# Performance work log

Hardware: AMD Instinct MI355X
Metric: run time of the kernel (lower is better)

## Reference

```python
import jax, jax.numpy as jnp
import numpy as np

L, B, S, E, H, V = 4, 2, 1024, 1024, 16, 32000
HD = E // H          # head_size = 64
FF = 6 * E           # FeedForward expansion = 6
EPS = 1e-5


def setup_inputs() -> dict:
    key = jax.random.key(0)
    ks = jax.random.split(key, 12)
    std = jnp.float32(0.02)

    def nrm(k, shape):
        return jax.random.normal(k, shape, jnp.float32) * std

    return {
        "x":   jax.random.randint(ks[0], (B, S), 0, V),
        "emb": nrm(ks[1], (V, E)),            # token embedding table
        "pos": nrm(ks[2], (S, E)),            # position embedding table (context = S)
        "Wq":  nrm(ks[3], (L, H, E, HD)),     # per-layer, per-head q Linear (no bias)
        "Wk":  nrm(ks[4], (L, H, E, HD)),
        "Wv":  nrm(ks[5], (L, H, E, HD)),
        "Wo":  nrm(ks[6], (L, E, E)),         # MHA output projection
        "g1":  jnp.ones((L, E), jnp.float32), "b1": jnp.zeros((L, E), jnp.float32),
        "g2":  jnp.ones((L, E), jnp.float32), "b2": jnp.zeros((L, E), jnp.float32),
        "W1":  nrm(ks[7], (L, E, FF)),        # FFN up
        "W2":  nrm(ks[8], (L, FF, E)),        # FFN down
        "gf":  jnp.ones((E,), jnp.float32), "bf": jnp.zeros((E,), jnp.float32),
        "Wf":  nrm(ks[9], (E, V)),            # final LM head (no bias)
    }


def _ln(x, g, b):
    mu = jnp.mean(x, -1, keepdims=True)
    var = jnp.mean((x - mu) ** 2, -1, keepdims=True)
    return (x - mu) * jax.lax.rsqrt(var + EPS) * g + b


def _gpt(x, emb, pos, Wq, Wk, Wv, Wo, g1, b1, g2, b2, W1, W2, gf, bf, Wf):
    Bsz, Sl = x.shape
    h = emb[x] + pos[:Sl]                         # [B,S,E]
    mask = jnp.tril(jnp.ones((Sl, Sl), bool))     # causal 'trill' buffer

    def block(h, p):
        wq, wk, wv, wo, ga, ba, gb, bb, w1, w2 = p
        z = _ln(h, ga, ba)
        q = jnp.einsum('bse,hed->bhsd', z, wq)
        k = jnp.einsum('bse,hed->bhsd', z, wk)
        v = jnp.einsum('bse,hed->bhsd', z, wv)
        att = jnp.einsum('bhsd,bhtd->bhst', q, k) * (HD ** -0.5)
        att = jnp.where(mask, att, -jnp.inf)
        att = jax.nn.softmax(att, axis=-1)
        o = jnp.einsum('bhst,bhtd->bhsd', att, v)
        o = o.transpose(0, 2, 1, 3).reshape(h.shape[0], h.shape[1], E)  # concat heads
        h = h + o @ wo                                                   # residual 1
        z = _ln(h, gb, bb)
        h = h + jax.nn.gelu(z @ w1, approximate=False) @ w2              # residual 2
        return h, None

    h, _ = jax.lax.scan(block, h, (Wq, Wk, Wv, Wo, g1, b1, g2, b2, W1, W2))
    return _ln(h, gf, bf) @ Wf                    # logits [B,S,V]


def reference(x, emb, pos, Wq, Wk, Wv, Wo, g1, b1, g2, b2, W1, W2, gf, bf, Wf):
    return _gpt(x, emb, pos, Wq, Wk, Wv, Wo, g1, b1, g2, b2, W1, W2, gf, bf, Wf)
```

## Files before the change

kernel.cpp:

```cpp
#include <hip/hip_runtime.h>
#include <hip/hip_bf16.h>
#include <math.h>


typedef unsigned short ushort_t;
typedef unsigned short us8 __attribute__((ext_vector_type(8)));
typedef unsigned short us4 __attribute__((ext_vector_type(4)));
typedef __bf16 bf16x8 __attribute__((ext_vector_type(8)));
typedef float f32x4 __attribute__((ext_vector_type(4)));

#define LN_EPS 1e-5f

__device__ inline ushort_t f2bf(float f) {
    union { float f; unsigned u; } v; v.f = f;
    unsigned r = v.u + 0x7FFFu + ((v.u >> 16) & 1u);
    return (ushort_t)(r >> 16);
}

#define GLD_LDS16(gp, lp)                                                  \
    __builtin_amdgcn_global_load_lds(                                      \
        (const __attribute__((address_space(1))) unsigned int*)(gp),       \
        (__attribute__((address_space(3))) unsigned int*)(lp), 16, 0, 0)

enum { EPI_F32 = 0, EPI_BF16 = 1, EPI_ADDF32 = 2, EPI_GELU = 3, EPI_TBF16 = 4,
       EPI_ATOM = 5, EPI_QKV = 6 };

template<int EPI>
__global__ __launch_bounds__(512)
void gemm8ph(const ushort_t* __restrict__ A, const ushort_t* __restrict__ B,
             void* __restrict__ Cv, int mt, int K, int lda, int ldb, int ldc)
{
    extern __shared__ ushort_t smem[];

    const int nwg  = gridDim.x;
    const int orig = blockIdx.x;
    int wgid = orig;
    if (nwg >= 8) {
        const int q = nwg >> 3, r = nwg & 7;
        const int xcd = orig & 7, i = orig >> 3;
        wgid = (xcd < r ? xcd * (q + 1) : r * (q + 1) + (xcd - r) * q) + i;
    }
    const int m0 = (wgid % mt) * 256;
    const int n0 = (wgid / mt) * 256;

    const int tid  = threadIdx.x;
    const int lane = tid & 63;
    const int wid  = tid >> 6;
    const int wm   = wid >> 2, wn = wid & 3;
    const int cg   = lane >> 4, cl = lane & 15;

    const int nt = K >> 6;
    const int ni = nt >> 1;

    auto stageA = [&](int t, int h) {
        ushort_t* dst = smem + (t & 1) * 32768 + h * 8192;
        const int k0 = t * 64;
        #pragma unroll
        for (int q = 0; q < 2; ++q) {
            const int slot = q * 512 + tid;
            const int r = slot >> 3, pc = slot & 7;
            const int col = (pc ^ (r & 7)) * 8;
            GLD_LDS16(&A[(long)(m0 + h * 128 + r) * lda + k0 + col], dst + slot * 8);
        }
    };
    auto stageB = [&](int t, int h) {
        ushort_t* dst = smem + (t & 1) * 32768 + 16384 + h * 8192;
        const int k0 = t * 64;
        #pragma unroll
        for (int q = 0; q < 2; ++q) {
            const int slot = q * 512 + tid;
            const int r = slot >> 3, pc = slot & 7;
            const int col = (pc ^ (r & 7)) * 8;
            GLD_LDS16(&B[(long)(n0 + h * 128 + r) * ldb + k0 + col], dst + slot * 8);
        }
    };

    stageA(0, 0); stageA(0, 1);
    stageB(0, 0); stageB(0, 1);
    stageB(1, 0); stageB(1, 1);
    asm volatile("s_waitcnt vmcnt(4)" ::: "memory");
    __builtin_amdgcn_s_barrier();

    f32x4 acc[8][4] = {};
    bf16x8 breg[4][2];

    for (int i = 0; i < ni; ++i) {
        const int te = 2 * i, to = te + 1;
        const bool nl = (i + 1 < ni);

        #pragma unroll
        for (int p = 0; p < 8; ++p) {
            const int t = (p < 4) ? te : to;
            const int q = p & 3;
            const ushort_t* Ar = smem + (t & 1) * 32768;
            const ushort_t* Br = Ar + 16384;

            if (q == 0) {
                #pragma unroll
                for (int nf = 0; nf < 4; ++nf) {
                    const int rb = wn * 64 + nf * 16 + cl;
                    #pragma unroll
                    for (int kk = 0; kk < 2; ++kk)
                        breg[nf][kk] = __builtin_bit_cast(bf16x8, *(const us8*)&Br[
                            rb * 64 + (((kk * 4 + cg) ^ (rb & 7)) * 8)]);
                }
            }
            bf16x8 af[2][2];
            #pragma unroll
            for (int mi = 0; mi < 2; ++mi) {
                const int ra = wm * 128 + q * 32 + mi * 16 + cl;
                #pragma unroll
                for (int kk = 0; kk < 2; ++kk)
                    af[mi][kk] = __builtin_bit_cast(bf16x8, *(const us8*)&Ar[
                        ra * 64 + (((kk * 4 + cg) ^ (ra & 7)) * 8)]);
            }

            if (p == 0)      { stageA(to, 0); }
            else if (p == 1) { stageA(to, 1); if (nl) stageB(te + 2, 0); }
            else if (p == 2) { if (nl) stageB(te + 2, 1); }
            else if (p == 4) { if (nl) stageA(te + 2, 0); }
            else if (p == 5) { if (nl) stageA(te + 2, 1); }
            else if (p == 6) { if (nl) stageB(to + 2, 0); }
            else if (p == 7) { if (nl) stageB(to + 2, 1); }

            __builtin_amdgcn_s_barrier();
            asm volatile("s_waitcnt lgkmcnt(0)" ::: "memory");
            __builtin_amdgcn_s_setprio(1);
            #pragma unroll
            for (int mi = 0; mi < 2; ++mi)
                #pragma unroll
                for (int nf = 0; nf < 4; ++nf)
                    #pragma unroll
                    for (int kk = 0; kk < 2; ++kk)
                        acc[q * 2 + mi][nf] = __builtin_amdgcn_mfma_f32_16x16x32_bf16(
                            af[mi][kk], breg[nf][kk], acc[q * 2 + mi][nf], 0, 0, 0);
            __builtin_amdgcn_s_setprio(0);

            if (p == 3) {
                if (nl) asm volatile("s_waitcnt vmcnt(4)" ::: "memory");
                else    asm volatile("s_waitcnt vmcnt(0)" ::: "memory");
            } else if (p == 7 && nl) {
                asm volatile("s_waitcnt vmcnt(4)" ::: "memory");
            }
            __builtin_amdgcn_s_barrier();
        }
    }

    const int rb = m0 + wm * 128 + cg * 4;
    const int cb = n0 + wn * 64 + cl;

    #pragma unroll
    for (int mf = 0; mf < 8; ++mf) {
        #pragma unroll
        for (int nf = 0; nf < 4; ++nf) {
            const int colg = cb + nf * 16;
            #pragma unroll
            for (int r = 0; r < 4; ++r) {
                const int  rowg = rb + mf * 16 + r;
                const long off  = (long)rowg * ldc + colg;
                const float val = acc[mf][nf][r];
                if (EPI == EPI_F32) {
                    ((float*)Cv)[off] = val;
                } else if (EPI == EPI_GELU) {
                    float g = 0.5f * val * (1.0f + erff(val * 0.70710678118654752f));
                    ((ushort_t*)Cv)[off] = f2bf(g);
                } else {
                    ((ushort_t*)Cv)[off] = f2bf(val);
                }
            }
        }
    }
}

template<int EPI>
__global__ __launch_bounds__(512)
void gemm8p(const ushort_t* __restrict__ A, const ushort_t* __restrict__ B,
            void* __restrict__ Cv, int mt, int K, int lda, int ldb, int ldc,
            long bsA, long bsB, long bsC)
{
    extern __shared__ ushort_t smem[];

    const int nwg  = gridDim.x;
    const int orig = blockIdx.x;
    int wgid = orig;
    if (nwg >= 8) {
        const int q = nwg >> 3, r = nwg & 7;
        const int xcd = orig & 7, i = orig >> 3;
        wgid = (xcd < r ? xcd * (q + 1) : r * (q + 1) + (xcd - r) * q) + i;
    }
    const int m0 = (wgid % mt) * 128;
    const int n0 = (wgid / mt) * 256;

    A += (long)blockIdx.z * bsA;
    B += (long)blockIdx.z * bsB;

    const int tid  = threadIdx.x;
    const int lane = tid & 63;
    const int wid  = tid >> 6;
    const int wm   = wid >> 2, wn = wid & 3;
    const int cg   = lane >> 4, cl = lane & 15;
    const int lr   = lane >> 3;
    const int lcc  = (lane & 7) * 8;

    const int nt = K >> 6;

    auto stage = [&](int kt, int buf, int part) {
        ushort_t* base = smem + buf * 24576;
        const int k0 = kt * 64;
        if (part < 2) {
            const int rbase = part * 64 + wid * 8;
            const int row   = rbase + lr;
            const int col   = lcc ^ ((row & 7) << 3);
            GLD_LDS16(&A[(long)(m0 + row) * lda + k0 + col], base + rbase * 64);
        } else {
            const int rbase = (part - 2) * 64 + wid * 8;
            const int row   = rbase + lr;
            const int col   = lcc ^ ((row & 7) << 3);
            GLD_LDS16(&B[(long)(n0 + row) * ldb + k0 + col],
                      base + 8192 + rbase * 64);
        }
    };

    #pragma unroll
    for (int p = 0; p < 6; ++p) stage(0, 0, p);
    #pragma unroll
    for (int p = 0; p < 6; ++p) stage(1, 1, p);
    asm volatile("s_waitcnt vmcnt(6)" ::: "memory");
    __builtin_amdgcn_s_barrier();

    f32x4 acc[4][4] = {};

    for (int t = 0; t < nt; ++t) {
        const ushort_t* Aq = smem + (t % 3) * 24576;
        const ushort_t* Bq = Aq + 8192;
        const int sbuf = (t + 2) % 3;
        const bool do_stage = (t + 2 < nt);

        bf16x8 breg[4][2];
        #pragma unroll
        for (int p = 0; p < 4; ++p) {
            const int rowA = wm * 64 + p * 16 + cl;
            bf16x8 aA[2];
            #pragma unroll
            for (int kk = 0; kk < 2; ++kk)
                aA[kk] = __builtin_bit_cast(bf16x8, *(const us8*)&Aq[
                    rowA * 64 + ((kk * 32 + cg * 8) ^ ((rowA & 7) << 3))]);
            if (p == 0) {
                #pragma unroll
                for (int nj = 0; nj < 4; ++nj) {
                    const int rowB = wn * 64 + nj * 16 + cl;
                    #pragma unroll
                    for (int kk = 0; kk < 2; ++kk)
                        breg[nj][kk] = __builtin_bit_cast(bf16x8, *(const us8*)&Bq[
                            rowB * 64 + ((kk * 32 + cg * 8) ^ ((rowB & 7) << 3))]);
                }
            }
            if (do_stage) {
                if (p == 0)      { stage(t + 2, sbuf, 0); stage(t + 2, sbuf, 1); }
                else if (p == 1) { stage(t + 2, sbuf, 2); stage(t + 2, sbuf, 3); }
                else if (p == 2) { stage(t + 2, sbuf, 4); }
                else             { stage(t + 2, sbuf, 5); }
            }
            __builtin_amdgcn_s_setprio(1);
            #pragma unroll
            for (int nj = 0; nj < 4; ++nj)
                #pragma unroll
                for (int kk = 0; kk < 2; ++kk)
                    acc[p][nj] = __builtin_amdgcn_mfma_f32_16x16x32_bf16(
                        aA[kk], breg[nj][kk], acc[p][nj], 0, 0, 0);
            __builtin_amdgcn_s_setprio(0);
            __builtin_amdgcn_s_barrier();
        }
        if (do_stage) asm volatile("s_waitcnt vmcnt(6)" ::: "memory");
        else          asm volatile("s_waitcnt vmcnt(0)" ::: "memory");
        __builtin_amdgcn_s_barrier();
    }

    const int rb = m0 + wm * 64 + cg * 4;
    const int cb = n0 + wn * 64 + cl;

    #pragma unroll
    for (int mi = 0; mi < 4; ++mi) {
        #pragma unroll
        for (int nj = 0; nj < 4; ++nj) {
            const int colg = cb + nj * 16;
            if (EPI == EPI_QKV) {
                ushort_t* Q = (ushort_t*)Cv;
                if (n0 < 1024) {
                    #pragma unroll
                    for (int r = 0; r < 4; ++r)
                        Q[(long)(rb + mi * 16 + r) * 1024 + colg] = f2bf(acc[mi][nj][r]);
                } else if (n0 < 2048) {
                    #pragma unroll
                    for (int r = 0; r < 4; ++r)
                        Q[2097152 + (long)(rb + mi * 16 + r) * 1024 + (colg - 1024)] =
                            f2bf(acc[mi][nj][r]);
                } else {
                    ushort_t* Vt = Q + 4194304;
                    const int rowg = rb + mi * 16;
                    const long boff = (long)(rowg >> 10) * 1048576;
                    us4 o4;
                    #pragma unroll
                    for (int r = 0; r < 4; ++r) o4[r] = f2bf(acc[mi][nj][r]);
                    *(us4*)&Vt[boff + (long)(colg - 2048) * 1024 + (rowg & 1023)] = o4;
                }
            } else {
                #pragma unroll
                for (int r = 0; r < 4; ++r) {
                    const int  rowg = rb + mi * 16 + r;
                    const long off  = (long)rowg * ldc + colg;
                    const float val = acc[mi][nj][r];
                    if (EPI == EPI_F32) {
                        ((float*)Cv)[off] = val;
                    } else if (EPI == EPI_GELU) {
                        float g = 0.5f * val * (1.0f + erff(val * 0.70710678118654752f));
                        ((ushort_t*)Cv)[off] = f2bf(g);
                    } else if (EPI == EPI_ATOM) {
                        atomicAdd(&((float*)Cv)[off], val);
                    } else {
                        ((ushort_t*)Cv)[off] = f2bf(val);
                    }
                }
            }
        }
    }
}

template<int EPI, int MT>
__global__ __launch_bounds__(256)
void gemm128(const ushort_t* __restrict__ A, const ushort_t* __restrict__ B,
             void* __restrict__ Cv, int K, int lda, int ldb, int ldc)
{
    const int m0 = blockIdx.x * (MT * 32);
    const int n0 = blockIdx.y * 128;

    __shared__ __align__(16) ushort_t As[MT * 32][64];
    __shared__ __align__(16) ushort_t Bs[128][64];

    const int tid  = threadIdx.x;
    const int lane = tid & 63;
    const int wid  = tid >> 6;
    const int wr   = wid >> 1, wc = wid & 1;
    const int lr   = lane >> 3;
    const int lc   = (lane & 7) * 8;
    const int cg   = lane >> 4;
    const int cl   = lane & 15;

    f32x4 acc[MT][4] = {};

    for (int k0 = 0; k0 < K; k0 += 64) {
        #pragma unroll
        for (int j = 0; j < MT; ++j) {
            const int r = wid * (8 * MT) + j * 8;
            GLD_LDS16(&A[(long)(m0 + r + lr) * lda + k0 + lc], &As[r][0]);
        }
        #pragma unroll
        for (int j = 0; j < 4; ++j) {
            const int r = wid * 32 + j * 8;
            GLD_LDS16(&B[(long)(n0 + r + lr) * ldb + k0 + lc], &Bs[r][0]);
        }
        __syncthreads();
        #pragma unroll
        for (int kk = 0; kk < 2; ++kk) {
            const int krd = kk * 32 + cg * 8;
            bf16x8 af[MT], bfr[4];
            #pragma unroll
            for (int mi = 0; mi < MT; ++mi)
                af[mi] = __builtin_bit_cast(bf16x8,
                    *(const us8*)&As[wr * (MT * 16) + mi * 16 + cl][krd]);
            #pragma unroll
            for (int nj = 0; nj < 4; ++nj)
                bfr[nj] = __builtin_bit_cast(bf16x8,
                    *(const us8*)&Bs[wc * 64 + nj * 16 + cl][krd]);
            #pragma unroll
            for (int mi = 0; mi < MT; ++mi)
                #pragma unroll
                for (int nj = 0; nj < 4; ++nj)
                    acc[mi][nj] = __builtin_amdgcn_mfma_f32_16x16x32_bf16(
                        af[mi], bfr[nj], acc[mi][nj], 0, 0, 0);
        }
        __syncthreads();
    }

    const int rb = m0 + wr * (MT * 16) + cg * 4;
    const int cb = n0 + wc * 64 + cl;

    #pragma unroll
    for (int mi = 0; mi < MT; ++mi)
        #pragma unroll
        for (int nj = 0; nj < 4; ++nj)
            #pragma unroll
            for (int r = 0; r < 4; ++r) {
                const long off = (long)(rb + mi * 16 + r) * ldc + cb + nj * 16;
                const float val = acc[mi][nj][r];
                if (EPI == EPI_ADDF32)      ((float*)Cv)[off] += val;
                else if (EPI == EPI_F32)    ((float*)Cv)[off] = val;
                else                        ((ushort_t*)Cv)[off] = f2bf(val);
            }
}

__global__ __launch_bounds__(256)
void flash_attn(const ushort_t* __restrict__ qb, const ushort_t* __restrict__ kb,
                const ushort_t* __restrict__ vT, ushort_t* __restrict__ ob)
{
    const int qt = gridDim.x - 1 - blockIdx.x;
    const int hh = blockIdx.y;
    const int bb = blockIdx.z;
    const int lane = threadIdx.x & 63;
    const int w    = threadIdx.x >> 6;
    const int cg   = lane >> 4;
    const int cl   = lane & 15;

    __shared__ __align__(16) ushort_t P_lds[4][16][72];

    const int q0 = qt * 64;
    const long tokQ = (long)bb * 1024 + q0 + w * 16 + cl;

    bf16x8 qf[2];
    #pragma unroll
    for (int kk = 0; kk < 2; ++kk)
        qf[kk] = __builtin_bit_cast(bf16x8,
            *(const us8*)&qb[tokQ * 1024 + hh * 64 + kk * 32 + cg * 8]);

    const ushort_t* kbase = kb + (long)bb * 1048576 + hh * 64;
    const ushort_t* vbase = vT + (long)bb * 1048576 + (long)hh * 65536;

    f32x4 o[4] = {};
    float m4[4], l4[4];
    #pragma unroll
    for (int r = 0; r < 4; ++r) { m4[r] = -1e30f; l4[r] = 0.0f; }

    for (int tt = 0; tt <= qt; ++tt) {
        const int t0 = tt * 64;
        f32x4 s[4] = {};
        __builtin_amdgcn_s_setprio(1);
        #pragma unroll
        for (int nj = 0; nj < 4; ++nj) {
            const ushort_t* kp = kbase + (long)(t0 + nj * 16 + cl) * 1024 + cg * 8;
            bf16x8 kf0 = __builtin_bit_cast(bf16x8, *(const us8*)kp);
            bf16x8 kf1 = __builtin_bit_cast(bf16x8, *(const us8*)(kp + 32));
            s[nj] = __builtin_amdgcn_mfma_f32_16x16x32_bf16(qf[0], kf0, s[nj], 0, 0, 0);
            s[nj] = __builtin_amdgcn_mfma_f32_16x16x32_bf16(qf[1], kf1, s[nj], 0, 0, 0);
        }
        __builtin_amdgcn_s_setprio(0);
        const bool diag = (tt == qt);
        float pm[4] = {-3e30f, -3e30f, -3e30f, -3e30f};
        #pragma unroll
        for (int nj = 0; nj < 4; ++nj)
            #pragma unroll
            for (int r = 0; r < 4; ++r) {
                float v = s[nj][r] * 0.125f;
                if (diag && (t0 + nj * 16 + cl) > (q0 + w * 16 + cg * 4 + r))
                    v = -1e30f;
                s[nj][r] = v;
                pm[r] = fmaxf(pm[r], v);
            }
        #pragma unroll
        for (int r = 0; r < 4; ++r)
            #pragma unroll
            for (int msk = 1; msk < 16; msk <<= 1)
                pm[r] = fmaxf(pm[r], __shfl_xor(pm[r], msk));
        float al[4], ps[4];
        #pragma unroll
        for (int r = 0; r < 4; ++r) {
            const float mn = fmaxf(m4[r], pm[r]);
            al[r] = __expf(m4[r] - mn);
            m4[r] = mn;
            ps[r] = 0.0f;
        }
        #pragma unroll
        for (int nj = 0; nj < 4; ++nj)
            #pragma unroll
            for (int r = 0; r < 4; ++r) {
                const float p = __expf(s[nj][r] - m4[r]);
                s[nj][r] = p;
                ps[r] += p;
            }
        #pragma unroll
        for (int r = 0; r < 4; ++r) {
            #pragma unroll
            for (int msk = 1; msk < 16; msk <<= 1)
                ps[r] += __shfl_xor(ps[r], msk);
            l4[r] = l4[r] * al[r] + ps[r];
        }
        #pragma unroll
        for (int nj = 0; nj < 4; ++nj)
            #pragma unroll
            for (int r = 0; r < 4; ++r) o[nj][r] *= al[r];
        #pragma unroll
        for (int nj = 0; nj < 4; ++nj)
            #pragma unroll
            for (int r = 0; r < 4; ++r)
                P_lds[w][cg * 4 + r][nj * 16 + cl] = f2bf(s[nj][r]);
        asm volatile("s_waitcnt lgkmcnt(0)" ::: "memory");
        __builtin_amdgcn_sched_barrier(0);
        bf16x8 pa[2];
        #pragma unroll
        for (int kk = 0; kk < 2; ++kk)
            pa[kk] = __builtin_bit_cast(bf16x8,
                *(const us8*)&P_lds[w][cl][kk * 32 + cg * 8]);
        __builtin_amdgcn_s_setprio(1);
        #pragma unroll
        for (int nj = 0; nj < 4; ++nj) {
            const ushort_t* vp = vbase + (long)(nj * 16 + cl) * 1024 + t0 + cg * 8;
            bf16x8 vf0 = __builtin_bit_cast(bf16x8, *(const us8*)vp);
            bf16x8 vf1 = __builtin_bit_cast(bf16x8, *(const us8*)(vp + 32));
            o[nj] = __builtin_amdgcn_mfma_f32_16x16x32_bf16(pa[0], vf0, o[nj], 0, 0, 0);
            o[nj] = __builtin_amdgcn_mfma_f32_16x16x32_bf16(pa[1], vf1, o[nj], 0, 0, 0);
        }
        __builtin_amdgcn_s_setprio(0);
    }

    #pragma unroll
    for (int r = 0; r < 4; ++r) {
        const float inv = 1.0f / l4[r];
        const long tok = (long)bb * 1024 + q0 + w * 16 + cg * 4 + r;
        #pragma unroll
        for (int nj = 0; nj < 4; ++nj)
            ob[tok * 1024 + hh * 64 + nj * 16 + cl] = f2bf(o[nj][r] * inv);
    }
}

__global__ __launch_bounds__(256)
void transpose_conv(const float* __restrict__ in, ushort_t* __restrict__ out,
                    long ldin, long ldout, long bsin, long bsout,
                    long bsout_hi, int zmod)
{
    __shared__ float tile[32][33];
    const int tx = threadIdx.x, ty = threadIdx.y;
    const long bin  = (long)blockIdx.z * bsin;
    const long bout = (long)(blockIdx.z % zmod) * bsout
                    + (long)(blockIdx.z / zmod) * bsout_hi;
    const int n0 = blockIdx.x * 32, k0 = blockIdx.y * 32;
    #pragma unroll
    for (int i = 0; i < 4; ++i)
        tile[ty + i * 8][tx] = in[bin + (long)(k0 + ty + i * 8) * ldin + n0 + tx];
    __syncthreads();
    #pragma unroll
    for (int i = 0; i < 4; ++i) {
        const int n = ty + i * 8;
        out[bout + (long)(n0 + n) * ldout + k0 + tx] = f2bf(tile[tx][n]);
    }
}

__global__ __launch_bounds__(256)
void embed_kernel(const int* __restrict__ x, const float* __restrict__ emb,
                  const float* __restrict__ pos, float* __restrict__ h)
{
    const int row = blockIdx.x, tid = threadIdx.x;
    const int s = row & 1023;
    const int idx = x[row];
    const float4 e = ((const float4*)(emb + (long)idx * 1024))[tid];
    const float4 p = ((const float4*)(pos + (long)s * 1024))[tid];
    float4 o; o.x = e.x + p.x; o.y = e.y + p.y; o.z = e.z + p.z; o.w = e.w + p.w;
    ((float4*)(h + (long)row * 1024))[tid] = o;
}

__global__ __launch_bounds__(256)
void ln_kernel(const float* __restrict__ x, const float* __restrict__ g,
               const float* __restrict__ b, ushort_t* __restrict__ z)
{
    const int row = blockIdx.x, tid = threadIdx.x;
    const float4 v = ((const float4*)(x + (long)row * 1024))[tid];
    float s  = v.x + v.y + v.z + v.w;
    float sq = v.x * v.x + v.y * v.y + v.z * v.z + v.w * v.w;
    #pragma unroll
    for (int o = 32; o > 0; o >>= 1) { s += __shfl_down(s, o); sq += __shfl_down(sq, o); }
    __shared__ float ls[4], lq[4];
    if ((tid & 63) == 0) { ls[tid >> 6] = s; lq[tid >> 6] = sq; }
    __syncthreads();
    s  = ls[0] + ls[1] + ls[2] + ls[3];
    sq = lq[0] + lq[1] + lq[2] + lq[3];
    const float mu   = s * (1.0f / 1024.0f);
    const float var  = sq * (1.0f / 1024.0f) - mu * mu;
    const float rstd = rsqrtf(var + LN_EPS);
    const float4 gg = ((const float4*)g)[tid];
    const float4 bb = ((const float4*)b)[tid];
    us4 o4;
    o4[0] = f2bf((v.x - mu) * rstd * gg.x + bb.x);
    o4[1] = f2bf((v.y - mu) * rstd * gg.y + bb.y);
    o4[2] = f2bf((v.z - mu) * rstd * gg.z + bb.z);
    o4[3] = f2bf((v.w - mu) * rstd * gg.w + bb.w);
    *(us4*)(z + (long)row * 1024 + tid * 4) = o4;
}

extern "C" void kernel_launch(void* const* d_in, const int* in_sizes, int n_in,
                              void* d_out, int out_size, void* d_ws, size_t ws_size,
                              hipStream_t stream)
{
    const int*   x   = (const int*)  d_in[0];
    const float* emb = (const float*)d_in[1];
    const float* pos = (const float*)d_in[2];
    const float* Wq  = (const float*)d_in[3];
    const float* Wk  = (const float*)d_in[4];
    const float* Wv  = (const float*)d_in[5];
    const float* Wo  = (const float*)d_in[6];
    const float* g1  = (const float*)d_in[7];
    const float* b1  = (const float*)d_in[8];
    const float* g2  = (const float*)d_in[9];
    const float* b2  = (const float*)d_in[10];
    const float* W1  = (const float*)d_in[11];
    const float* W2  = (const float*)d_in[12];
    const float* gf  = (const float*)d_in[13];
    const float* bfp = (const float*)d_in[14];
    const float* Wf  = (const float*)d_in[15];
    float* out = (float*)d_out;

    char* ws = (char*)d_ws;
    size_t off = 0;
    auto alloc = [&](size_t bytes) {
        char* p = ws + off;
        off = (off + bytes + 255) & ~(size_t)255;
        return p;
    };
    ushort_t* WqkvT = (ushort_t*)alloc(4UL * 3145728 * 2);
    ushort_t* WoT   = (ushort_t*)alloc(4UL * 1048576 * 2);
    ushort_t* W1T   = (ushort_t*)alloc(4UL * 6291456 * 2);
    ushort_t* W2T   = (ushort_t*)alloc(4UL * 6291456 * 2);
    ushort_t* WfT   = (ushort_t*)alloc(32768000UL * 2);
    float*    h     = (float*)   alloc(2048UL * 1024 * 4);
    ushort_t* z     = (ushort_t*)alloc(2048UL * 1024 * 2);
    ushort_t* qb    = (ushort_t*)alloc(3UL * 2048 * 1024 * 2);
    ushort_t* kb    = qb + 2097152;
    ushort_t* vT    = qb + 4194304;
    ushort_t* ob    = (ushort_t*)alloc(2048UL * 1024 * 2);
    ushort_t* ub    = (ushort_t*)alloc(2048UL * 6144 * 2);
    (void)ws_size; (void)in_sizes; (void)n_in; (void)out_size;

    const int LDS8P = 2 * 32768 * 2;
    const int LDS3B = 3 * 49152;
    hipFuncSetAttribute((const void*)&gemm8ph<EPI_F32>,
                        hipFuncAttributeMaxDynamicSharedMemorySize, LDS8P);
    hipFuncSetAttribute((const void*)&gemm8ph<EPI_GELU>,
                        hipFuncAttributeMaxDynamicSharedMemorySize, LDS8P);
    hipFuncSetAttribute((const void*)&gemm8p<EPI_QKV>,
                        hipFuncAttributeMaxDynamicSharedMemorySize, LDS3B);
    hipFuncSetAttribute((const void*)&gemm8p<EPI_ATOM>,
                        hipFuncAttributeMaxDynamicSharedMemorySize, LDS3B);

    const dim3 tb(32, 8);
    transpose_conv<<<dim3(2,   32, 64), tb, 0, stream>>>(Wq, WqkvT,           64, 1024, 65536, 65536, 3145728, 16);
    transpose_conv<<<dim3(2,   32, 64), tb, 0, stream>>>(Wk, WqkvT + 1048576, 64, 1024, 65536, 65536, 3145728, 16);
    transpose_conv<<<dim3(2,   32, 64), tb, 0, stream>>>(Wv, WqkvT + 2097152, 64, 1024, 65536, 65536, 3145728, 16);
    transpose_conv<<<dim3(32,  32,  4), tb, 0, stream>>>(Wo, WoT, 1024,  1024, 1048576, 1048576, 0, 4);
    transpose_conv<<<dim3(192, 32,  4), tb, 0, stream>>>(W1, W1T, 6144,  1024, 6291456, 6291456, 0, 4);
    transpose_conv<<<dim3(32, 192,  4), tb, 0, stream>>>(W2, W2T, 1024,  6144, 6291456, 6291456, 0, 4);
    transpose_conv<<<dim3(1000,32,  1), tb, 0, stream>>>(Wf, WfT, 32000, 1024, 0,       0,       0, 1);

    embed_kernel<<<2048, 256, 0, stream>>>(x, emb, pos, h);

    for (int l = 0; l < 4; ++l) {
        const size_t wff = (size_t)l * 6291456;

        ln_kernel<<<2048, 256, 0, stream>>>(h, g1 + l * 1024, b1 + l * 1024, z);

        gemm8p<EPI_QKV><<<dim3(16 * 12), 512, LDS3B, stream>>>(
            z, WqkvT + (size_t)l * 3145728, qb, 16, 1024, 1024, 1024, 1024, 0, 0, 0);

        flash_attn<<<dim3(16, 16, 2), 256, 0, stream>>>(qb, kb, vT, ob);

        gemm128<EPI_ADDF32, 2><<<dim3(32, 8), 256, 0, stream>>>(
            ob, WoT + (size_t)l * 1048576, h, 1024, 1024, 1024, 1024);

        ln_kernel<<<2048, 256, 0, stream>>>(h, g2 + l * 1024, b2 + l * 1024, z);

        gemm8ph<EPI_GELU><<<dim3(8 * 24), 512, LDS8P, stream>>>(
            z, W1T + wff, ub, 8, 1024, 1024, 1024, 6144);
        gemm8p<EPI_ATOM><<<dim3(16 * 4, 1, 4), 512, LDS3B, stream>>>(
            ub, W2T + wff, h, 16, 1536, 6144, 6144, 1024, 1536, 1536, 0);
    }

    ln_kernel<<<2048, 256, 0, stream>>>(h, gf, bfp, z);
    gemm8ph<EPI_F32><<<dim3(8 * 125), 512, LDS8P, stream>>>(
        z, WfT, out, 8, 1024, 1024, 1024, 32000);
}
```

Baseline: 1.173 ms.

## Software-pipeline LDS fragment reads one phase ahead with double-buffered A registers

Reads the A fragments for the next phase (and B fragments for the next k-tile) from LDS while the current phase's MFMAs run, using ping-pong register buffers. The LDS wait before the MFMAs becomes a partial lgkmcnt, and one barrier per phase is removed. The global-load vmcnt waits move one phase earlier to match. The aim is to hide LDS read latency behind matrix math, at the cost of more registers and fragile wait-count and barrier ordering that could race with the stage writes into LDS.

Result: slower. 1.403 ms (median of 4 runs) (+19.6%).

```diff
diff --git a/kernel.cpp b/kernel.cpp
--- a/kernel.cpp
+++ b/kernel.cpp
@@ -74,6 +74,28 @@
             GLD_LDS16(&B[(long)(n0 + h * 128 + r) * ldb + k0 + col], dst + slot * 8);
         }
     };
+    auto readA = [&](int t, int q, bf16x8 (&af)[2][2]) {
+        const ushort_t* Ar = smem + (t & 1) * 32768;
+        #pragma unroll
+        for (int mi = 0; mi < 2; ++mi) {
+            const int ra = wm * 128 + q * 32 + mi * 16 + cl;
+            #pragma unroll
+            for (int kk = 0; kk < 2; ++kk)
+                af[mi][kk] = __builtin_bit_cast(bf16x8, *(const us8*)&Ar[
+                    ra * 64 + (((kk * 4 + cg) ^ (ra & 7)) * 8)]);
+        }
+    };
+    auto readB = [&](int t, bf16x8 (&bg)[4][2]) {
+        const ushort_t* Br = smem + (t & 1) * 32768 + 16384;
+        #pragma unroll
+        for (int nf = 0; nf < 4; ++nf) {
+            const int rb = wn * 64 + nf * 16 + cl;
+            #pragma unroll
+            for (int kk = 0; kk < 2; ++kk)
+                bg[nf][kk] = __builtin_bit_cast(bf16x8, *(const us8*)&Br[
+                    rb * 64 + (((kk * 4 + cg) ^ (rb & 7)) * 8)]);
+        }
+    };
 
     stageA(0, 0); stageA(0, 1);
     stageB(0, 0); stageB(0, 1);
@@ -81,8 +103,12 @@
     asm volatile("s_waitcnt vmcnt(4)" ::: "memory");
     __builtin_amdgcn_s_barrier();
 
+    bf16x8 afA[2][2], afB[2][2];
+    bf16x8 breg[4][2];
+    readA(0, 0, afA);
+    readB(0, breg);
+
     f32x4 acc[8][4] = {};
-    bf16x8 breg[4][2];
 
     for (int i = 0; i < ni; ++i) {
         const int te = 2 * i, to = te + 1;
@@ -90,29 +116,17 @@
 
         #pragma unroll
         for (int p = 0; p < 8; ++p) {
-            const int t = (p < 4) ? te : to;
             const int q = p & 3;
-            const ushort_t* Ar = smem + (t & 1) * 32768;
-            const ushort_t* Br = Ar + 16384;
-
-            if (q == 0) {
-                #pragma unroll
-                for (int nf = 0; nf < 4; ++nf) {
-                    const int rb = wn * 64 + nf * 16 + cl;
-                    #pragma unroll
-                    for (int kk = 0; kk < 2; ++kk)
-                        breg[nf][kk] = __builtin_bit_cast(bf16x8, *(const us8*)&Br[
-                            rb * 64 + (((kk * 4 + cg) ^ (rb & 7)) * 8)]);
-                }
-            }
-            bf16x8 af[2][2];
-            #pragma unroll
-            for (int mi = 0; mi < 2; ++mi) {
-                const int ra = wm * 128 + q * 32 + mi * 16 + cl;
-                #pragma unroll
-                for (int kk = 0; kk < 2; ++kk)
-                    af[mi][kk] = __builtin_bit_cast(bf16x8, *(const us8*)&Ar[
-                        ra * 64 + (((kk * 4 + cg) ^ (ra & 7)) * 8)]);
+            const bool have_next = !(p == 7 && !nl);
+
+            if (have_next) {
+                int nat, naq;
+                if (p < 3)       { nat = te;     naq = p + 1; }
+                else if (p == 3) { nat = to;     naq = 0;     }
+                else if (p < 7)  { nat = to;     naq = p - 3; }
+                else             { nat = te + 2; naq = 0;     }
+                if (p & 1) readA(nat, naq, afA);
+                else       readA(nat, naq, afB);
             }
 
             if (p == 0)      { stageA(to, 0); }
@@ -123,8 +137,10 @@
             else if (p == 6) { if (nl) stageB(to + 2, 0); }
             else if (p == 7) { if (nl) stageB(to + 2, 1); }
 
-            __builtin_amdgcn_s_barrier();
-            asm volatile("s_waitcnt lgkmcnt(0)" ::: "memory");
+            if (have_next) asm volatile("s_waitcnt lgkmcnt(4)" ::: "memory");
+            else           asm volatile("s_waitcnt lgkmcnt(0)" ::: "memory");
+            __builtin_amdgcn_sched_barrier(0);
+
             __builtin_amdgcn_s_setprio(1);
             #pragma unroll
             for (int mi = 0; mi < 2; ++mi)
@@ -133,14 +149,18 @@
                     #pragma unroll
                     for (int kk = 0; kk < 2; ++kk)
                         acc[q * 2 + mi][nf] = __builtin_amdgcn_mfma_f32_16x16x32_bf16(
-                            af[mi][kk], breg[nf][kk], acc[q * 2 + mi][nf], 0, 0, 0);
+                            (p & 1) ? afB[mi][kk] : afA[mi][kk],
+                            breg[nf][kk], acc[q * 2 + mi][nf], 0, 0, 0);
             __builtin_amdgcn_s_setprio(0);
 
-            if (p == 3) {
+            if (p == 3)            readB(to, breg);
+            else if (p == 7 && nl) readB(te + 2, breg);
+
+            if (p == 2) {
                 if (nl) asm volatile("s_waitcnt vmcnt(4)" ::: "memory");
                 else    asm volatile("s_waitcnt vmcnt(0)" ::: "memory");
-            } else if (p == 7 && nl) {
-                asm volatile("s_waitcnt vmcnt(4)" ::: "memory");
+            } else if (p == 6 && nl) {
+                asm volatile("s_waitcnt vmcnt(2)" ::: "memory");
             }
             __builtin_amdgcn_s_barrier();
         }
```
